# Kernel optimization log

Hardware: AMD Instinct MI355X
Metric: run time of the kernel (lower is better)

The kernel has to match this reference:

```python
import jax, jax.numpy as jnp
import numpy as np

SEQ_LS = [512, 512, 512, 512]
HEADS = 8
DIM_HEAD = 64
DIM = 512
INNER = HEADS * DIM_HEAD  # 512
N = sum(SEQ_LS)           # 2048
B = 4
EPS = 1e-5

# static modality id per token position: [N]
MOD_IDS = jnp.asarray(np.repeat(np.arange(len(SEQ_LS)), SEQ_LS))


def setup_inputs() -> dict:
    key = jax.random.key(0)
    ks = jax.random.split(key, 6)
    x = jax.random.normal(ks[0], (B, N, DIM), dtype=jnp.float32)
    m_labels = jnp.ones((B, len(SEQ_LS)), dtype=jnp.int64 if jax.config.jax_enable_x64 else jnp.int32)
    gamma = jnp.ones((DIM,), dtype=jnp.float32)
    beta = jnp.zeros((DIM,), dtype=jnp.float32)
    w_qkv = jax.random.normal(ks[1], (DIM, 3 * INNER), dtype=jnp.float32) * (DIM ** -0.5)
    w_out = jax.random.normal(ks[2], (INNER, DIM), dtype=jnp.float32) * (INNER ** -0.5)
    b_out = jnp.zeros((DIM,), dtype=jnp.float32)
    return {"x": x, "m_labels": m_labels, "gamma": gamma, "beta": beta,
            "w_qkv": w_qkv, "w_out": w_out, "b_out": b_out}


def _additive_mask(m_labels):
    # present[b, n] = modality of token n is present in sample b
    present = (m_labels[:, MOD_IDS] != 0)                       # [B, N] bool
    pair_ok = present[:, :, None] & present[:, None, :]         # [B, N, N]
    neg_inf = jnp.float32(-jnp.inf)
    return jnp.where(pair_ok, jnp.float32(0.0), neg_inf)        # [B, N, N]


def reference(x, m_labels, gamma, beta, w_qkv, w_out, b_out):
    # LayerNorm(dim)
    mu = jnp.mean(x, axis=-1, keepdims=True)
    var = jnp.mean(jnp.square(x - mu), axis=-1, keepdims=True)
    xn = (x - mu) * jax.lax.rsqrt(var + EPS) * gamma + beta

    # QKV projection (no bias), split heads
    qkv = jnp.einsum('bnd,de->bne', xn, w_qkv)                  # [B, N, 3*INNER]
    q, k, v = jnp.split(qkv, 3, axis=-1)
    def heads(t):
        return t.reshape(B, N, HEADS, DIM_HEAD).transpose(0, 2, 1, 3)  # [B, H, N, Dh]
    q, k, v = heads(q), heads(k), heads(v)

    scale = DIM_HEAD ** -0.5
    dots = jnp.einsum('bhnd,bhmd->bhnm', q, k) * scale          # [B, H, N, N]
    dots = dots + _additive_mask(m_labels)[:, None, :, :]
    attn = jax.nn.softmax(dots, axis=-1)
    out = jnp.einsum('bhnm,bhmd->bhnd', attn, v)                # [B, H, N, Dh]
    out = out.transpose(0, 2, 1, 3).reshape(B, N, INNER)        # [B, N, INNER]
    return jnp.einsum('bni,io->bno', out, w_out) + b_out        # [B, N, DIM]
```

## Files before the change

kernel.cpp:

```cpp
#include <hip/hip_runtime.h>

#define DIMD 512
#define NTOK 2048
#define HEADS 8
#define DH 64

typedef __attribute__((ext_vector_type(4))) float f32x4;
typedef __attribute__((ext_vector_type(8))) __bf16 bf16x8;
typedef __attribute__((ext_vector_type(4))) short s16x4;

#define MFMA16(a, b, c) __builtin_amdgcn_mfma_f32_16x16x32_bf16((a), (b), (c), 0, 0, 0)
#define MFMAK16(a, b, c) __builtin_amdgcn_mfma_f32_16x16x16bf16_1k((a), (b), (c), 0, 0, 0)

__device__ __forceinline__ unsigned short f2bf(float f) {
  unsigned int u = __float_as_uint(f);
  u += 0x7fffu + ((u >> 16) & 1u);
  return (unsigned short)(u >> 16);
}

__device__ __forceinline__ unsigned packhi(float b, float a) {
#if __has_builtin(__builtin_amdgcn_perm)
  return __builtin_amdgcn_perm(__float_as_uint(a), __float_as_uint(b), 0x07060302u);
#else
  return (__float_as_uint(b) >> 16) | (__float_as_uint(a) & 0xffff0000u);
#endif
}

__device__ __forceinline__ void gl2lds16(const void* g, void* l) {
  auto gp = reinterpret_cast<__attribute__((address_space(1))) unsigned int*>(
      reinterpret_cast<unsigned long long>(g));
  auto lp = reinterpret_cast<__attribute__((address_space(3))) unsigned int*>(
      reinterpret_cast<unsigned long long>(l));
  __builtin_amdgcn_global_load_lds(gp, lp, 16, 0, 0);
}

__global__ __launch_bounds__(256) void prep_kernel(const float* __restrict__ x,
                                                   const float* __restrict__ gamma,
                                                   const float* __restrict__ beta,
                                                   const float* __restrict__ w_qkv,
                                                   const float* __restrict__ w_out,
                                                   unsigned short* __restrict__ xn,
                                                   unsigned short* __restrict__ wqkvT,
                                                   unsigned short* __restrict__ woutT) {
  __shared__ float t[32][33];
  const int bid = blockIdx.x;
  if (bid < 2048) {
    const int row = bid * 4 + (threadIdx.x >> 6);
    const int lane = threadIdx.x & 63;
    const float4* xr = (const float4*)(x + (size_t)row * DIMD);
    float4 a = xr[lane];
    float4 b = xr[lane + 64];
    float s = a.x + a.y + a.z + a.w + b.x + b.y + b.z + b.w;
    for (int off = 1; off < 64; off <<= 1) s += __shfl_xor(s, off, 64);
    float mu = s * (1.0f / DIMD);
    float d0 = a.x - mu, d1 = a.y - mu, d2 = a.z - mu, d3 = a.w - mu;
    float e0 = b.x - mu, e1 = b.y - mu, e2 = b.z - mu, e3 = b.w - mu;
    float v = d0 * d0 + d1 * d1 + d2 * d2 + d3 * d3 + e0 * e0 + e1 * e1 + e2 * e2 + e3 * e3;
    for (int off = 1; off < 64; off <<= 1) v += __shfl_xor(v, off, 64);
    float rs = rsqrtf(v * (1.0f / DIMD) + 1e-5f);
    const float4* g4 = (const float4*)gamma;
    const float4* be4 = (const float4*)beta;
    float4 ga = g4[lane], gb = g4[lane + 64];
    float4 ba = be4[lane], bb = be4[lane + 64];
    unsigned p0 = (unsigned)f2bf(d0 * rs * ga.x + ba.x) | ((unsigned)f2bf(d1 * rs * ga.y + ba.y) << 16);
    unsigned p1 = (unsigned)f2bf(d2 * rs * ga.z + ba.z) | ((unsigned)f2bf(d3 * rs * ga.w + ba.w) << 16);
    unsigned p2 = (unsigned)f2bf(e0 * rs * gb.x + bb.x) | ((unsigned)f2bf(e1 * rs * gb.y + bb.y) << 16);
    unsigned p3 = (unsigned)f2bf(e2 * rs * gb.z + bb.z) | ((unsigned)f2bf(e3 * rs * gb.w + bb.w) << 16);
    uint2 w0; w0.x = p0; w0.y = p1;
    uint2 w1; w1.x = p2; w1.y = p3;
    *(uint2*)&xn[(size_t)row * DIMD + lane * 4] = w0;
    *(uint2*)&xn[(size_t)row * DIMD + 256 + lane * 4] = w1;
  } else {
    const float* w;
    unsigned short* wt;
    int C, bx, by;
    if (bid < 2816) { w = w_qkv; wt = wqkvT; C = 1536; bx = (bid - 2048) % 48; by = (bid - 2048) / 48; }
    else            { w = w_out; wt = woutT; C = 512;  bx = (bid - 2816) % 16; by = (bid - 2816) / 16; }
    const int R = 512;
    int tx = threadIdx.x & 31, ty = threadIdx.x >> 5;
    int c0 = bx * 32, r0 = by * 32;
    for (int i = 0; i < 4; i++)
      t[ty + 8 * i][tx] = w[(size_t)(r0 + ty + 8 * i) * C + c0 + tx];
    __syncthreads();
    for (int i = 0; i < 4; i++)
      wt[(size_t)(c0 + ty + 8 * i) * R + r0 + tx] = f2bf(t[tx][ty + 8 * i]);
  }
}

__global__ __launch_bounds__(256, 2) void qkv_gemm(const unsigned short* __restrict__ A,
                                                   const unsigned short* __restrict__ Bt,
                                                   unsigned short* __restrict__ qb,
                                                   unsigned short* __restrict__ kb,
                                                   unsigned short* __restrict__ vtb) {
  __shared__ unsigned short As[2][128 * 64];
  __shared__ unsigned short Bs[2][128 * 64];
  const int tid = threadIdx.x;
  const int wave = tid >> 6, lane = tid & 63;
  const int row16 = lane & 15, quad = lane >> 4;
  const int rho = row16 & 7;
  const int m0 = blockIdx.x * 128;
  const int n0 = blockIdx.y * 128;
  const int rw = (wave & 1) * 64, cw = (wave >> 1) * 64;

  const char* Ab = (const char*)A;
  const char* Bb = (const char*)Bt;
#pragma unroll
  for (int i = 0; i < 4; i++) {
    int idx = i * 256 + tid;
    int r = idx >> 3;
    int c = (idx & 7) ^ (r & 7);
    gl2lds16(Ab + ((size_t)(m0 + r) * DIMD) * 2 + c * 16, (char*)As[0] + idx * 16);
    gl2lds16(Bb + ((size_t)(n0 + r) * DIMD) * 2 + c * 16, (char*)Bs[0] + idx * 16);
  }
  __syncthreads();

  f32x4 acc[4][4] = {};
  for (int kt = 0; kt < 8; kt++) {
    const int buf = kt & 1;
    if (kt < 7) {
      const int k0 = (kt + 1) * 64;
#pragma unroll
      for (int i = 0; i < 4; i++) {
        int idx = i * 256 + tid;
        int r = idx >> 3;
        int c = (idx & 7) ^ (r & 7);
        gl2lds16(Ab + ((size_t)(m0 + r) * DIMD + k0) * 2 + c * 16, (char*)As[buf ^ 1] + idx * 16);
        gl2lds16(Bb + ((size_t)(n0 + r) * DIMD + k0) * 2 + c * 16, (char*)Bs[buf ^ 1] + idx * 16);
      }
    }
#pragma unroll
    for (int ks = 0; ks < 2; ks++) {
      bf16x8 av[4], bv[4];
#pragma unroll
      for (int i = 0; i < 4; i++) {
        int Ra = rw + i * 16 + row16;
        int Rb = cw + i * 16 + row16;
        av[i] = *(const bf16x8*)&As[buf][Ra * 64 + (((ks * 4 + quad) ^ rho) * 8)];
        bv[i] = *(const bf16x8*)&Bs[buf][Rb * 64 + (((ks * 4 + quad) ^ rho) * 8)];
      }
#pragma unroll
      for (int i = 0; i < 4; i++)
#pragma unroll
        for (int j = 0; j < 4; j++) acc[i][j] = MFMA16(av[i], bv[j], acc[i][j]);
    }
    __syncthreads();
  }

  unsigned short* Ct = (unsigned short*)As;
#pragma unroll
  for (int i = 0; i < 4; i++)
#pragma unroll
    for (int j = 0; j < 4; j++)
#pragma unroll
      for (int r = 0; r < 4; r++)
        Ct[(rw + i * 16 + quad * 4 + r) * 136 + cw + j * 16 + row16] = f2bf(acc[i][j][r]);
  __syncthreads();

  const int sect = n0 >> 9;
  const int h0 = (n0 & 511) >> 6;
  const int b = m0 >> 11;
  const int nbase = m0 & 2047;
  if (sect < 2) {
    unsigned short* dst = (sect == 0) ? qb : kb;
#pragma unroll
    for (int i = 0; i < 8; i++) {
      int cid = i * 256 + tid;
      int row = cid >> 4, col0 = (cid & 15) * 8;
      int h = h0 + (col0 >> 6), d0 = col0 & 63;
      uint4 val = *(const uint4*)&Ct[row * 136 + col0];
      *(uint4*)&dst[(((size_t)(b * HEADS + h) * NTOK) + nbase + row) * DH + d0] = val;
    }
  } else {
#pragma unroll
    for (int u = 0; u < 4; u++) {
      int uid = u * 256 + tid;
      int col = uid >> 3, rc = (uid & 7) * 16;
      int h = h0 + (col >> 6), d = col & 63;
      unsigned short tmp[16];
#pragma unroll
      for (int j = 0; j < 16; j++) tmp[j] = Ct[(rc + j) * 136 + col];
      size_t base = ((size_t)(b * HEADS + h) * DH + d) * NTOK + nbase + rc;
      *(uint4*)&vtb[base] = *(uint4*)&tmp[0];
      *(uint4*)&vtb[base + 8] = *(uint4*)&tmp[8];
    }
  }
}

__global__ __launch_bounds__(512) void attn_kernel(const unsigned short* __restrict__ qb,
                                                   const unsigned short* __restrict__ kb,
                                                   const unsigned short* __restrict__ vtb,
                                                   const int* __restrict__ mlab,
                                                   unsigned short* __restrict__ ao) {
  __shared__ unsigned short Qs[256 * 64];
  __shared__ unsigned short Ks[2][64 * 64];
  __shared__ unsigned short Vs[2][64 * 64];
  const int tid = threadIdx.x;
  const int wave = tid >> 6, lane = tid & 63;
  const int row16 = lane & 15, quad = lane >> 4;
  const int rho = row16 & 7;
  const int bh = blockIdx.y;
  const int b = bh >> 3, h = bh & 7;
  const int q0 = blockIdx.x * 256;

  const char* qg = (const char*)(qb + ((size_t)bh * NTOK + q0) * DH);
  const char* kgb = (const char*)(kb + (size_t)bh * NTOK * DH);
  const char* vgb = (const char*)(vtb + (size_t)bh * DH * NTOK);
  const int sr = tid >> 3;
  const int sc = (tid & 7) ^ (sr & 7);

#pragma unroll
  for (int i = 0; i < 4; i++)
    gl2lds16(qg + (sr + 64 * i) * 128 + sc * 16, (char*)Qs + tid * 16 + i * 8192);
  gl2lds16(kgb + sr * 128 + sc * 16, (char*)Ks[0] + tid * 16);
  gl2lds16(vgb + (size_t)sr * 4096 + sc * 16, (char*)Vs[0] + tid * 16);
  __syncthreads();

  bf16x8 aq[2][2];
#pragma unroll
  for (int qs = 0; qs < 2; qs++) {
    const int qrow = wave * 32 + qs * 16 + row16;
#pragma unroll
    for (int ki = 0; ki < 2; ki++)
      aq[qs][ki] = *(const bf16x8*)&Qs[qrow * 64 + (((ki * 4 + quad) ^ rho) * 8)];
  }

  f32x4 accT[4][2] = {};
  float lsum[2] = {0.f, 0.f};
  const float cs = 0.125f * 1.44269504088896f;
  const float c0 = mlab[b * 4 + 0] ? -16.f : -100000.f;
  const float c1 = mlab[b * 4 + 1] ? -16.f : -100000.f;
  const float c2 = mlab[b * 4 + 2] ? -16.f : -100000.f;
  const float c3 = mlab[b * 4 + 3] ? -16.f : -100000.f;

  for (int t = 0; t < 32; t++) {
    const int buf = t & 1;
    if (t < 31) {
      gl2lds16(kgb + (size_t)(t + 1) * 8192 + sr * 128 + sc * 16, (char*)Ks[buf ^ 1] + tid * 16);
      gl2lds16(vgb + (size_t)(t + 1) * 128 + (size_t)sr * 4096 + sc * 16, (char*)Vs[buf ^ 1] + tid * 16);
    }
    f32x4 S[2][4];
#pragma unroll
    for (int f = 0; f < 4; f++) {
      const unsigned short* Kr = &Ks[buf][(f * 16 + row16) * 64];
      bf16x8 ak0 = *(const bf16x8*)&Kr[(quad ^ rho) * 8];
      bf16x8 ak1 = *(const bf16x8*)&Kr[((quad + 4) ^ rho) * 8];
#pragma unroll
      for (int qs = 0; qs < 2; qs++) {
        f32x4 z = {};
        z = MFMA16(ak0, aq[qs][0], z);
        z = MFMA16(ak1, aq[qs][1], z);
        S[qs][f] = z;
      }
    }
    const int mi = t >> 3;
    const float c = (mi == 0) ? c0 : (mi == 1) ? c1 : (mi == 2) ? c2 : c3;
    s16x4 pf[2][4];
#pragma unroll
    for (int qs = 0; qs < 2; qs++)
#pragma unroll
      for (int f = 0; f < 4; f++) {
        float p0 = exp2f(fmaf(S[qs][f][0], cs, c));
        float p1 = exp2f(fmaf(S[qs][f][1], cs, c));
        float p2 = exp2f(fmaf(S[qs][f][2], cs, c));
        float p3 = exp2f(fmaf(S[qs][f][3], cs, c));
        lsum[qs] += (p0 + p1) + (p2 + p3);
        uint2 pk;
        pk.x = packhi(p0, p1);
        pk.y = packhi(p2, p3);
        pf[qs][f] = *(s16x4*)&pk;
      }
#pragma unroll
    for (int g = 0; g < 4; g++) {
      const unsigned short* Vr = &Vs[buf][(g * 16 + row16) * 64];
#pragma unroll
      for (int u = 0; u < 4; u++) {
        s16x4 va = *(const s16x4*)&Vr[(((2 * u + (quad >> 1)) ^ rho) * 8) + (quad & 1) * 4];
#pragma unroll
        for (int qs = 0; qs < 2; qs++) accT[g][qs] = MFMAK16(va, pf[qs][u], accT[g][qs]);
      }
    }
    __syncthreads();
  }

#pragma unroll
  for (int qs = 0; qs < 2; qs++) {
    float s = lsum[qs];
    s += __shfl_xor(s, 16, 64);
    s += __shfl_xor(s, 32, 64);
    lsum[qs] = 1.0f / s;
  }
#pragma unroll
  for (int qs = 0; qs < 2; qs++) {
    const int q = q0 + wave * 32 + qs * 16 + row16;
    unsigned short* aor = ao + ((size_t)b * NTOK + q) * DIMD + h * DH;
#pragma unroll
    for (int g = 0; g < 4; g++) {
      *(unsigned*)&aor[g * 16 + quad * 4] = packhi(accT[g][qs][0] * lsum[qs], accT[g][qs][1] * lsum[qs]);
      *(unsigned*)&aor[g * 16 + quad * 4 + 2] = packhi(accT[g][qs][2] * lsum[qs], accT[g][qs][3] * lsum[qs]);
    }
  }
}

__global__ __launch_bounds__(256, 2) void out_gemm(const unsigned short* __restrict__ A,
                                                   const unsigned short* __restrict__ Bt,
                                                   const float* __restrict__ bias,
                                                   float* __restrict__ out) {
  __shared__ unsigned short As[2][128 * 64];
  __shared__ unsigned short Bs[2][64 * 64];
  const int tid = threadIdx.x;
  const int wave = tid >> 6, lane = tid & 63;
  const int row16 = lane & 15, quad = lane >> 4;
  const int rho = row16 & 7;
  const int m0 = blockIdx.x * 128;
  const int n0 = blockIdx.y * 64;
  const int rw = (wave & 1) * 64, cw = (wave >> 1) * 32;

  const char* Ab = (const char*)A;
  const char* Bb = (const char*)Bt;
#pragma unroll
  for (int i = 0; i < 4; i++) {
    int idx = i * 256 + tid;
    int r = idx >> 3;
    int c = (idx & 7) ^ (r & 7);
    gl2lds16(Ab + ((size_t)(m0 + r) * DIMD) * 2 + c * 16, (char*)As[0] + idx * 16);
  }
#pragma unroll
  for (int i = 0; i < 2; i++) {
    int idx = i * 256 + tid;
    int r = idx >> 3;
    int c = (idx & 7) ^ (r & 7);
    gl2lds16(Bb + ((size_t)(n0 + r) * DIMD) * 2 + c * 16, (char*)Bs[0] + idx * 16);
  }
  __syncthreads();

  f32x4 acc[4][2] = {};
  for (int kt = 0; kt < 8; kt++) {
    const int buf = kt & 1;
    if (kt < 7) {
      const int k0 = (kt + 1) * 64;
#pragma unroll
      for (int i = 0; i < 4; i++) {
        int idx = i * 256 + tid;
        int r = idx >> 3;
        int c = (idx & 7) ^ (r & 7);
        gl2lds16(Ab + ((size_t)(m0 + r) * DIMD + k0) * 2 + c * 16, (char*)As[buf ^ 1] + idx * 16);
      }
#pragma unroll
      for (int i = 0; i < 2; i++) {
        int idx = i * 256 + tid;
        int r = idx >> 3;
        int c = (idx & 7) ^ (r & 7);
        gl2lds16(Bb + ((size_t)(n0 + r) * DIMD + k0) * 2 + c * 16, (char*)Bs[buf ^ 1] + idx * 16);
      }
    }
#pragma unroll
    for (int ks = 0; ks < 2; ks++) {
      bf16x8 av[4], bv[2];
#pragma unroll
      for (int i = 0; i < 4; i++)
        av[i] = *(const bf16x8*)&As[buf][(rw + i * 16 + row16) * 64 + (((ks * 4 + quad) ^ rho) * 8)];
#pragma unroll
      for (int j = 0; j < 2; j++)
        bv[j] = *(const bf16x8*)&Bs[buf][(cw + j * 16 + row16) * 64 + (((ks * 4 + quad) ^ rho) * 8)];
#pragma unroll
      for (int i = 0; i < 4; i++)
#pragma unroll
        for (int j = 0; j < 2; j++) acc[i][j] = MFMA16(av[i], bv[j], acc[i][j]);
    }
    __syncthreads();
  }

#pragma unroll
  for (int j = 0; j < 2; j++) {
    const int col = n0 + cw + j * 16 + row16;
    const float bv = bias[col];
#pragma unroll
    for (int i = 0; i < 4; i++)
#pragma unroll
      for (int r = 0; r < 4; r++) {
        const int row = m0 + rw + i * 16 + quad * 4 + r;
        out[(size_t)row * DIMD + col] = acc[i][j][r] + bv;
      }
  }
}

extern "C" void kernel_launch(void* const* d_in, const int* in_sizes, int n_in,
                              void* d_out, int out_size, void* d_ws, size_t ws_size,
                              hipStream_t stream) {
  const float* x = (const float*)d_in[0];
  const int* mlab = (const int*)d_in[1];
  const float* gamma = (const float*)d_in[2];
  const float* beta = (const float*)d_in[3];
  const float* w_qkv = (const float*)d_in[4];
  const float* w_out = (const float*)d_in[5];
  const float* b_out = (const float*)d_in[6];
  float* out = (float*)d_out;

  char* ws = (char*)d_ws;
  unsigned short* xn = (unsigned short*)(ws);
  unsigned short* wqkvT = (unsigned short*)(ws + 8388608);
  unsigned short* woutT = (unsigned short*)(ws + 9961472);
  unsigned short* qbuf = (unsigned short*)(ws + 10485760);
  unsigned short* kbuf = (unsigned short*)(ws + 18874368);
  unsigned short* vtbuf = (unsigned short*)(ws + 27262976);
  unsigned short* aobuf = (unsigned short*)(ws + 35651584);

  prep_kernel<<<3072, 256, 0, stream>>>(x, gamma, beta, w_qkv, w_out, xn, wqkvT, woutT);
  qkv_gemm<<<dim3(64, 12), 256, 0, stream>>>(xn, wqkvT, qbuf, kbuf, vtbuf);
  attn_kernel<<<dim3(8, 32), 512, 0, stream>>>(qbuf, kbuf, vtbuf, mlab, aobuf);
  out_gemm<<<dim3(64, 8), 256, 0, stream>>>(aobuf, woutT, b_out, out);
}
```

Measured before the change: 166.6 us.

## Switch GEMM and attention loads to triple-buffered LDS with partial vmcnt waits

Replaces double buffering with a three-stage LDS ring in the QKV GEMM, attention and output GEMM kernels, prefetching two tiles ahead. A single s_waitcnt vmcnt(N) plus s_barrier at the top of each iteration replaces the full __syncthreads at the end, so the next tile's loads stay in flight during compute. The cost is more LDS per block, which may lower occupancy (the min-blocks launch bound is dropped), and correctness depends on hand-counted vmcnt values and on the compiler not reordering the async loads.

```diff
diff --git a/kernel.cpp b/kernel.cpp
--- a/kernel.cpp
+++ b/kernel.cpp
@@ -11,6 +11,8 @@
 
 #define MFMA16(a, b, c) __builtin_amdgcn_mfma_f32_16x16x32_bf16((a), (b), (c), 0, 0, 0)
 #define MFMAK16(a, b, c) __builtin_amdgcn_mfma_f32_16x16x16bf16_1k((a), (b), (c), 0, 0, 0)
+
+#define WAIT_BAR(N) asm volatile("s_waitcnt vmcnt(" #N ")\n\ts_barrier" ::: "memory")
 
 __device__ __forceinline__ unsigned short f2bf(float f) {
   unsigned int u = __float_as_uint(f);
@@ -87,13 +89,13 @@
   }
 }
 
-__global__ __launch_bounds__(256, 2) void qkv_gemm(const unsigned short* __restrict__ A,
-                                                   const unsigned short* __restrict__ Bt,
-                                                   unsigned short* __restrict__ qb,
-                                                   unsigned short* __restrict__ kb,
-                                                   unsigned short* __restrict__ vtb) {
-  __shared__ unsigned short As[2][128 * 64];
-  __shared__ unsigned short Bs[2][128 * 64];
+__global__ __launch_bounds__(256) void qkv_gemm(const unsigned short* __restrict__ A,
+                                                const unsigned short* __restrict__ Bt,
+                                                unsigned short* __restrict__ qb,
+                                                unsigned short* __restrict__ kb,
+                                                unsigned short* __restrict__ vtb) {
+  __shared__ unsigned short As[3][128 * 64];
+  __shared__ unsigned short Bs[3][128 * 64];
   const int tid = threadIdx.x;
   const int wave = tid >> 6, lane = tid & 63;
   const int row16 = lane & 15, quad = lane >> 4;
@@ -105,29 +107,32 @@
   const char* Ab = (const char*)A;
   const char* Bb = (const char*)Bt;
 #pragma unroll
-  for (int i = 0; i < 4; i++) {
-    int idx = i * 256 + tid;
-    int r = idx >> 3;
-    int c = (idx & 7) ^ (r & 7);
-    gl2lds16(Ab + ((size_t)(m0 + r) * DIMD) * 2 + c * 16, (char*)As[0] + idx * 16);
-    gl2lds16(Bb + ((size_t)(n0 + r) * DIMD) * 2 + c * 16, (char*)Bs[0] + idx * 16);
-  }
-  __syncthreads();
+  for (int kt = 0; kt < 2; kt++)
+#pragma unroll
+    for (int i = 0; i < 4; i++) {
+      int idx = i * 256 + tid;
+      int r = idx >> 3;
+      int c = (idx & 7) ^ (r & 7);
+      gl2lds16(Ab + ((size_t)(m0 + r) * DIMD + kt * 64) * 2 + c * 16, (char*)As[kt] + idx * 16);
+      gl2lds16(Bb + ((size_t)(n0 + r) * DIMD + kt * 64) * 2 + c * 16, (char*)Bs[kt] + idx * 16);
+    }
 
   f32x4 acc[4][4] = {};
   for (int kt = 0; kt < 8; kt++) {
-    const int buf = kt & 1;
-    if (kt < 7) {
-      const int k0 = (kt + 1) * 64;
+    if (kt == 7) WAIT_BAR(0); else WAIT_BAR(8);
+    if (kt < 6) {
+      const int k0 = (kt + 2) * 64;
+      const int buf2 = (kt + 2) % 3;
 #pragma unroll
       for (int i = 0; i < 4; i++) {
         int idx = i * 256 + tid;
         int r = idx >> 3;
         int c = (idx & 7) ^ (r & 7);
-        gl2lds16(Ab + ((size_t)(m0 + r) * DIMD + k0) * 2 + c * 16, (char*)As[buf ^ 1] + idx * 16);
-        gl2lds16(Bb + ((size_t)(n0 + r) * DIMD + k0) * 2 + c * 16, (char*)Bs[buf ^ 1] + idx * 16);
-      }
-    }
+        gl2lds16(Ab + ((size_t)(m0 + r) * DIMD + k0) * 2 + c * 16, (char*)As[buf2] + idx * 16);
+        gl2lds16(Bb + ((size_t)(n0 + r) * DIMD + k0) * 2 + c * 16, (char*)Bs[buf2] + idx * 16);
+      }
+    }
+    const int buf = kt % 3;
 #pragma unroll
     for (int ks = 0; ks < 2; ks++) {
       bf16x8 av[4], bv[4];
@@ -143,8 +148,8 @@
 #pragma unroll
         for (int j = 0; j < 4; j++) acc[i][j] = MFMA16(av[i], bv[j], acc[i][j]);
     }
-    __syncthreads();
-  }
+  }
+  __syncthreads();
 
   unsigned short* Ct = (unsigned short*)As;
 #pragma unroll
@@ -192,8 +197,8 @@
                                                    const int* __restrict__ mlab,
                                                    unsigned short* __restrict__ ao) {
   __shared__ unsigned short Qs[256 * 64];
-  __shared__ unsigned short Ks[2][64 * 64];
-  __shared__ unsigned short Vs[2][64 * 64];
+  __shared__ unsigned short Ks[3][64 * 64];
+  __shared__ unsigned short Vs[3][64 * 64];
   const int tid = threadIdx.x;
   const int wave = tid >> 6, lane = tid & 63;
   const int row16 = lane & 15, quad = lane >> 4;
@@ -213,7 +218,9 @@
     gl2lds16(qg + (sr + 64 * i) * 128 + sc * 16, (char*)Qs + tid * 16 + i * 8192);
   gl2lds16(kgb + sr * 128 + sc * 16, (char*)Ks[0] + tid * 16);
   gl2lds16(vgb + (size_t)sr * 4096 + sc * 16, (char*)Vs[0] + tid * 16);
-  __syncthreads();
+  gl2lds16(kgb + 8192 + sr * 128 + sc * 16, (char*)Ks[1] + tid * 16);
+  gl2lds16(vgb + 128 + (size_t)sr * 4096 + sc * 16, (char*)Vs[1] + tid * 16);
+  WAIT_BAR(4);
 
   bf16x8 aq[2][2];
 #pragma unroll
@@ -233,11 +240,12 @@
   const float c3 = mlab[b * 4 + 3] ? -16.f : -100000.f;
 
   for (int t = 0; t < 32; t++) {
-    const int buf = t & 1;
-    if (t < 31) {
-      gl2lds16(kgb + (size_t)(t + 1) * 8192 + sr * 128 + sc * 16, (char*)Ks[buf ^ 1] + tid * 16);
-      gl2lds16(vgb + (size_t)(t + 1) * 128 + (size_t)sr * 4096 + sc * 16, (char*)Vs[buf ^ 1] + tid * 16);
-    }
+    if (t == 31) WAIT_BAR(0); else WAIT_BAR(2);
+    if (t < 30) {
+      gl2lds16(kgb + (size_t)(t + 2) * 8192 + sr * 128 + sc * 16, (char*)Ks[(t + 2) % 3] + tid * 16);
+      gl2lds16(vgb + (size_t)(t + 2) * 128 + (size_t)sr * 4096 + sc * 16, (char*)Vs[(t + 2) % 3] + tid * 16);
+    }
+    const int buf = t % 3;
     f32x4 S[2][4];
 #pragma unroll
     for (int f = 0; f < 4; f++) {
@@ -279,7 +287,6 @@
         for (int qs = 0; qs < 2; qs++) accT[g][qs] = MFMAK16(va, pf[qs][u], accT[g][qs]);
       }
     }
-    __syncthreads();
   }
 
 #pragma unroll
@@ -301,12 +308,12 @@
   }
 }
 
-__global__ __launch_bounds__(256, 2) void out_gemm(const unsigned short* __restrict__ A,
-                                                   const unsigned short* __restrict__ Bt,
-                                                   const float* __restrict__ bias,
-                                                   float* __restrict__ out) {
-  __shared__ unsigned short As[2][128 * 64];
-  __shared__ unsigned short Bs[2][64 * 64];
+__global__ __launch_bounds__(256) void out_gemm(const unsigned short* __restrict__ A,
+                                                const unsigned short* __restrict__ Bt,
+                                                const float* __restrict__ bias,
+                                                float* __restrict__ out) {
+  __shared__ unsigned short As[3][128 * 64];
+  __shared__ unsigned short Bs[3][64 * 64];
   const int tid = threadIdx.x;
   const int wave = tid >> 6, lane = tid & 63;
   const int row16 = lane & 15, quad = lane >> 4;
@@ -318,41 +325,45 @@
   const char* Ab = (const char*)A;
   const char* Bb = (const char*)Bt;
 #pragma unroll
-  for (int i = 0; i < 4; i++) {
-    int idx = i * 256 + tid;
-    int r = idx >> 3;
-    int c = (idx & 7) ^ (r & 7);
-    gl2lds16(Ab + ((size_t)(m0 + r) * DIMD) * 2 + c * 16, (char*)As[0] + idx * 16);
-  }
-#pragma unroll
-  for (int i = 0; i < 2; i++) {
-    int idx = i * 256 + tid;
-    int r = idx >> 3;
-    int c = (idx & 7) ^ (r & 7);
-    gl2lds16(Bb + ((size_t)(n0 + r) * DIMD) * 2 + c * 16, (char*)Bs[0] + idx * 16);
-  }
-  __syncthreads();
+  for (int kt = 0; kt < 2; kt++) {
+#pragma unroll
+    for (int i = 0; i < 4; i++) {
+      int idx = i * 256 + tid;
+      int r = idx >> 3;
+      int c = (idx & 7) ^ (r & 7);
+      gl2lds16(Ab + ((size_t)(m0 + r) * DIMD + kt * 64) * 2 + c * 16, (char*)As[kt] + idx * 16);
+    }
+#pragma unroll
+    for (int i = 0; i < 2; i++) {
+      int idx = i * 256 + tid;
+      int r = idx >> 3;
+      int c = (idx & 7) ^ (r & 7);
+      gl2lds16(Bb + ((size_t)(n0 + r) * DIMD + kt * 64) * 2 + c * 16, (char*)Bs[kt] + idx * 16);
+    }
+  }
 
   f32x4 acc[4][2] = {};
   for (int kt = 0; kt < 8; kt++) {
-    const int buf = kt & 1;
-    if (kt < 7) {
-      const int k0 = (kt + 1) * 64;
+    if (kt == 7) WAIT_BAR(0); else WAIT_BAR(6);
+    if (kt < 6) {
+      const int k0 = (kt + 2) * 64;
+      const int buf2 = (kt + 2) % 3;
 #pragma unroll
       for (int i = 0; i < 4; i++) {
         int idx = i * 256 + tid;
         int r = idx >> 3;
         int c = (idx & 7) ^ (r & 7);
-        gl2lds16(Ab + ((size_t)(m0 + r) * DIMD + k0) * 2 + c * 16, (char*)As[buf ^ 1] + idx * 16);
+        gl2lds16(Ab + ((size_t)(m0 + r) * DIMD + k0) * 2 + c * 16, (char*)As[buf2] + idx * 16);
       }
 #pragma unroll
       for (int i = 0; i < 2; i++) {
         int idx = i * 256 + tid;
         int r = idx >> 3;
         int c = (idx & 7) ^ (r & 7);
-        gl2lds16(Bb + ((size_t)(n0 + r) * DIMD + k0) * 2 + c * 16, (char*)Bs[buf ^ 1] + idx * 16);
-      }
-    }
+        gl2lds16(Bb + ((size_t)(n0 + r) * DIMD + k0) * 2 + c * 16, (char*)Bs[buf2] + idx * 16);
+      }
+    }
+    const int buf = kt % 3;
 #pragma unroll
     for (int ks = 0; ks < 2; ks++) {
       bf16x8 av[4], bv[2];
@@ -367,7 +378,6 @@
 #pragma unroll
         for (int j = 0; j < 2; j++) acc[i][j] = MFMA16(av[i], bv[j], acc[i][j]);
     }
-    __syncthreads();
   }
 
 #pragma unroll
```

Measured after the change: 169.5 us. No clear change (+1.7%).
